# Kernel tuning notes

Measured on AMD Instinct MI355X. Metric: run time of the kernel, lower is better.

## Reference

```python
import jax, jax.numpy as jnp
import numpy as np

B = 128          # batch of codewords
M_CHK = 288      # n_check_nodes
N_VAR = 576      # n_variable_nodes
K_INFO = 288     # n_information_bits
N_ITER = 5
EDGE_P = 0.02    # ~11-12 edges per check row, LDPC-like sparsity


def setup_inputs() -> dict:
    key = jax.random.key(0)
    k1, k2, k3, k4 = jax.random.split(key, 4)
    inputs = jax.random.normal(k1, (B, N_VAR), dtype=jnp.float32)
    # sparse binary parity-check matrix, batched (keras RNN constants carry batch dim)
    H = jax.random.bernoulli(k2, EDGE_P, (B, M_CHK, N_VAR)).astype(jnp.float32)
    sigma2 = 0.5 + 0.5 * jax.random.uniform(k3, (B, 1), dtype=jnp.float32)
    # learned parameters
    input_ponderation = jnp.ones((N_ITER, 1), dtype=jnp.float32)
    out_ponderation = jnp.ones((N_ITER, 1), dtype=jnp.float32)
    skip_ponderation = jnp.ones((1, 1), dtype=jnp.float32)
    # per-edge check-to-variable weights of the neural BP cell
    w_cv = 1.0 + 0.02 * jax.random.normal(k4, (M_CHK, N_VAR), dtype=jnp.float32)
    gate_logit = jnp.asarray(0.0, dtype=jnp.float32)
    return {"inputs": inputs, "H": H, "sigma2": sigma2,
            "input_ponderation": input_ponderation,
            "out_ponderation": out_ponderation,
            "skip_ponderation": skip_ponderation,
            "w_cv": w_cv, "gate_logit": gate_logit}


def _decode(inputs, H, sigma2, input_ponderation, out_ponderation,
            skip_ponderation, w_cv, gate_logit):
    llrs = -4.0 * inputs / sigma2                                    # [B, n]
    # trainable=True path: normalize by mean |llr|
    norm_llrs = llrs / jnp.mean(jnp.abs(llrs), axis=-1, keepdims=True)
    # tile over iterations and apply input ponderation -> [B, T, n]
    x = norm_llrs[:, None, :] * input_ponderation

    mask = H                                                         # [B, m, n]
    gate = jax.nn.sigmoid(gate_logit)

    def cell(Mstate, x_t):
        # variable-to-check extrinsic messages on edges
        S = jnp.sum(Mstate, axis=1, keepdims=True)                   # [B, 1, n]
        V = (x_t[:, None, :] + S - Mstate) * mask                    # [B, m, n]
        # tanh-product check-node update (product excluding self via divide)
        t = jnp.tanh(0.5 * jnp.clip(V, -15.0, 15.0))
        t_edge = jnp.where(mask > 0, t, 1.0)
        P = jnp.prod(t_edge, axis=-1, keepdims=True)                 # [B, m, 1]
        t_safe = jnp.where(jnp.abs(t_edge) < 1e-7,
                           jnp.where(t_edge >= 0, 1e-7, -1e-7), t_edge)
        r = jnp.clip(P / t_safe, -1.0 + 1e-6, 1.0 - 1e-6)
        M_new = 2.0 * jnp.arctanh(r) * w_cv * mask                   # weighted c2v
        # gated (damped) state update
        M_out = gate * M_new + (1.0 - gate) * Mstate
        posterior = x_t + jnp.sum(M_out, axis=1)                     # [B, n]
        return M_out, posterior

    M0 = jnp.zeros_like(H)
    xs = jnp.swapaxes(x, 0, 1)                                       # [T, B, n]
    _, posts = jax.lax.scan(cell, M0, xs)
    outputs = jnp.swapaxes(posts, 0, 1)                              # [B, T, n]

    # post-normalization per iteration, weighted pooling over iterations
    norm_out = outputs / jnp.mean(jnp.abs(outputs), axis=-1, keepdims=True)
    pooled = jnp.mean(out_ponderation * norm_out, axis=-2)           # [B, n]
    out = pooled + skip_ponderation * norm_llrs                      # [1,1] broadcast
    return jax.nn.sigmoid(-out[:, :K_INFO])


def reference(inputs, H, sigma2, input_ponderation, out_ponderation,
              skip_ponderation, w_cv, gate_logit):
    return _decode(inputs, H, sigma2, input_ponderation, out_ponderation,
                   skip_ponderation, w_cv, gate_logit)
```

## Files before the change

### kernel.cpp

```cpp
#include <hip/hip_runtime.h>
#include <hip/hip_bf16.h>

#define B_SZ 128
#define MCHK 288
#define NVAR 576
#define KINFO 288
#define NITER 5
#define CAP 40
#define LCAP 3712
#define TPB 1024

__global__ __launch_bounds__(256) void build_edges(const float* __restrict__ H,
                                                   int* __restrict__ cntG,
                                                   unsigned short* __restrict__ idxG) {
    int row  = blockIdx.x * 4 + (threadIdx.x >> 6);
    int lane = threadIdx.x & 63;
    const float* hrow = H + (size_t)row * NVAR;
    const float4* h4  = (const float4*)hrow;
    float4 a = h4[lane];
    float4 bq = h4[64 + lane];
    float  c = hrow[512 + lane];
    int cnt = (a.x!=0.f)+(a.y!=0.f)+(a.z!=0.f)+(a.w!=0.f)
            + (bq.x!=0.f)+(bq.y!=0.f)+(bq.z!=0.f)+(bq.w!=0.f) + (c!=0.f);
    int pre = cnt;
    #pragma unroll
    for (int o = 1; o < 64; o <<= 1) {
        int n = __shfl_up(pre, o, 64);
        if (lane >= o) pre += n;
    }
    int p = pre - cnt;
    unsigned short* dst = idxG + (size_t)row * CAP;
    int base = lane * 4;
    if (a.x!=0.f)  { if (p<CAP) dst[p] = (unsigned short)(base    ); p++; }
    if (a.y!=0.f)  { if (p<CAP) dst[p] = (unsigned short)(base + 1); p++; }
    if (a.z!=0.f)  { if (p<CAP) dst[p] = (unsigned short)(base + 2); p++; }
    if (a.w!=0.f)  { if (p<CAP) dst[p] = (unsigned short)(base + 3); p++; }
    if (bq.x!=0.f) { if (p<CAP) dst[p] = (unsigned short)(256 + base    ); p++; }
    if (bq.y!=0.f) { if (p<CAP) dst[p] = (unsigned short)(256 + base + 1); p++; }
    if (bq.z!=0.f) { if (p<CAP) dst[p] = (unsigned short)(256 + base + 2); p++; }
    if (bq.w!=0.f) { if (p<CAP) dst[p] = (unsigned short)(256 + base + 3); p++; }
    if (c!=0.f)    { if (p<CAP) dst[p] = (unsigned short)(512 + lane);     p++; }
    if (lane == 63) cntG[row] = (pre > CAP) ? CAP : pre;
}

__global__ __launch_bounds__(TPB) void decode(
    const float* __restrict__ inp,   const float* __restrict__ sigma2,
    const float* __restrict__ ipond, const float* __restrict__ opond,
    const float* __restrict__ skipp, const float* __restrict__ wcv,
    const float* __restrict__ gatel, const int* __restrict__ cntG,
    const unsigned short* __restrict__ idxG, float* __restrict__ out) {

    __shared__ float xln[NVAR];
    __shared__ float S[NVAR];
    __shared__ float pooled[NVAR];
    __shared__ float Prow[MCHK];
    __shared__ float Mld[LCAP];
    __shared__ float tld[LCAP];
    __shared__ unsigned int ev[LCAP];
    __shared__ int   rcnt[MCHK];
    __shared__ int   roff[MCHK];
    __shared__ float red[16];
    __shared__ float scal;
    __shared__ int   EtotS;

    const int b    = blockIdx.x;
    const int tid  = threadIdx.x;
    const int wid  = tid >> 6;
    const int lane = tid & 63;

    const float sig  = sigma2[b];
    const float gate = 1.0f / (1.0f + __expf(-gatel[0]));
    const float gbar = 1.0f - gate;
    const float skip = skipp[0];

    float l = 0.0f, al = 0.0f;
    if (tid < NVAR) { l = -4.0f * inp[(size_t)b * NVAR + tid] / sig; al = fabsf(l); }
    #pragma unroll
    for (int o = 32; o; o >>= 1) al += __shfl_down(al, o, 64);
    if (lane == 0) red[wid] = al;

    int* sc = (int*)tld;
    if (tid < 512) {
        int cc = 0;
        if (tid < MCHK) { cc = cntG[b * MCHK + tid]; rcnt[tid] = cc; }
        sc[tid] = cc;
    }
    __syncthreads();
    if (tid == 0) {
        float s = 0.0f;
        #pragma unroll
        for (int i = 0; i < 16; ++i) s += red[i];
        scal = (float)NVAR / s;
    }
    __syncthreads();
    if (tid < NVAR) {
        xln[tid]    = l * scal;
        pooled[tid] = 0.0f;
        S[tid]      = 0.0f;
    }
    for (int d = 1; d < 512; d <<= 1) {
        int v = 0;
        if (tid < 512) v = sc[tid] + ((tid >= d) ? sc[tid - d] : 0);
        __syncthreads();
        if (tid < 512) sc[tid] = v;
        __syncthreads();
    }
    if (tid < MCHK) {
        int c = rcnt[tid];
        int o = sc[tid] - c;
        if (o >= LCAP)            { o = 0; c = 0; }
        else if (o + c > LCAP)    { c = LCAP - o; }
        roff[tid] = o; rcnt[tid] = c;
        const unsigned short* ig = idxG + ((size_t)b * MCHK + tid) * CAP;
        for (int j = 0; j < c; ++j) {
            int v = ig[j];
            ev[o + j]  = ((unsigned)tid << 16) | (unsigned)v;
            Mld[o + j] = 0.0f;
        }
    }
    if (tid == 0) EtotS = (sc[MCHK - 1] > LCAP) ? LCAP : sc[MCHK - 1];
    __syncthreads();
    const int E = EtotS;

    float ipl[NITER], opl[NITER];
    #pragma unroll
    for (int t = 0; t < NITER; ++t) { ipl[t] = ipond[t]; opl[t] = opond[t]; }

    for (int t = 0; t < NITER; ++t) {
        const float pt = ipl[t], ot = opl[t];

        for (int e = tid; e < E; e += TPB) {
            int v   = (int)(ev[e] & 0xFFFFu);
            float V = fmaf(pt, xln[v], S[v]) - Mld[e];
            V = fminf(15.0f, fmaxf(-15.0f, V));
            float ex = __expf(V);
            float te = (ex - 1.0f) * __builtin_amdgcn_rcpf(ex + 1.0f);
            float x  = 0.5f * V, x2 = x * x;
            float tp = x * fmaf(x2, fmaf(x2, fmaf(x2, -0.05396825f, 0.13333333f),
                                         -0.33333333f), 1.0f);
            tld[e] = (fabsf(V) < 0.5f) ? tp : te;
        }
        __syncthreads();

        if (tid < MCHK) {
            int c = rcnt[tid], o = roff[tid];
            float P = 1.0f;
            for (int j = 0; j < c; ++j) P *= tld[o + j];
            Prow[tid] = P;
        }
        if (tid < NVAR) S[tid] = 0.0f;
        __syncthreads();

        for (int e = tid; e < E; e += TPB) {
            unsigned pk = ev[e];
            int v = (int)(pk & 0xFFFFu);
            int m = (int)(pk >> 16);
            float tj = tld[e];
            float ts = (fabsf(tj) < 1e-7f) ? ((tj >= 0.0f) ? 1e-7f : -1e-7f) : tj;
            float r  = Prow[m] * __builtin_amdgcn_rcpf(ts);
            r = fminf(1.0f - 1e-6f, fmaxf(-1.0f + 1e-6f, r));
            float w  = wcv[m * NVAR + v];
            float Mn = __logf((1.0f + r) * __builtin_amdgcn_rcpf(1.0f - r)) * w;
            float Mo = fmaf(gate, Mn, gbar * Mld[e]);
            Mld[e] = Mo;
            atomicAdd(&S[v], Mo);
        }
        __syncthreads();

        float post = 0.0f, ap = 0.0f;
        if (tid < NVAR) { post = fmaf(pt, xln[tid], S[tid]); ap = fabsf(post); }
        #pragma unroll
        for (int o = 32; o; o >>= 1) ap += __shfl_down(ap, o, 64);
        if (lane == 0) red[wid] = ap;
        __syncthreads();
        if (tid == 0) {
            float s2 = 0.0f;
            #pragma unroll
            for (int i = 0; i < 16; ++i) s2 += red[i];
            scal = (float)NVAR / s2;
        }
        __syncthreads();
        if (tid < NVAR) pooled[tid] += ot * post * scal;
    }

    if (tid < KINFO) {
        float o = pooled[tid] * (1.0f / NITER) + skip * xln[tid];
        out[(size_t)b * KINFO + tid] = 1.0f / (1.0f + __expf(o));
    }
}

extern "C" void kernel_launch(void* const* d_in, const int* in_sizes, int n_in,
                              void* d_out, int out_size, void* d_ws, size_t ws_size,
                              hipStream_t stream) {
    const float* inp    = (const float*)d_in[0];
    const float* H      = (const float*)d_in[1];
    const float* sigma2 = (const float*)d_in[2];
    const float* ipond  = (const float*)d_in[3];
    const float* opond  = (const float*)d_in[4];
    const float* skipp  = (const float*)d_in[5];
    const float* wcv    = (const float*)d_in[6];
    const float* gatel  = (const float*)d_in[7];
    float* out = (float*)d_out;

    int* cntG = (int*)d_ws;
    unsigned short* idxG =
        (unsigned short*)((char*)d_ws + (size_t)B_SZ * MCHK * sizeof(int));

    build_edges<<<(B_SZ * MCHK) / 4, 256, 0, stream>>>(H, cntG, idxG);
    decode<<<B_SZ, TPB, 0, stream>>>(inp, sigma2, ipond, opond, skipp,
                                     wcv, gatel, cntG, idxG, out);
}
```

Before: 172.2 us.

## Split each codeword across two blocks with grid barrier and fused edge extraction

Removes the separate edge-building kernel and extracts edges from H inside the decode kernel using wave ballots, caching per-edge w_cv weights in shared memory. Each codeword's check rows are split across two blocks (256 blocks total), which exchange partial variable sums through global memory each iteration via a two-level grid-wide atomic barrier. This aims to double parallelism and cut launch and global gather costs. It relies on all 256 blocks being co-resident to avoid deadlock and adds barrier latency every iteration.

Result: slower. 254.8 us (+47.9%).

```diff
diff --git a/kernel.cpp b/kernel.cpp
--- a/kernel.cpp
+++ b/kernel.cpp
@@ -1,137 +1,126 @@
 #include <hip/hip_runtime.h>
-#include <hip/hip_bf16.h>
-
-#define B_SZ 128
-#define MCHK 288
-#define NVAR 576
+
+#define B_SZ  128
+#define MCHK  288
+#define NVAR  576
 #define KINFO 288
 #define NITER 5
-#define CAP 40
-#define LCAP 3712
-#define TPB 1024
-
-__global__ __launch_bounds__(256) void build_edges(const float* __restrict__ H,
-                                                   int* __restrict__ cntG,
-                                                   unsigned short* __restrict__ idxG) {
-    int row  = blockIdx.x * 4 + (threadIdx.x >> 6);
-    int lane = threadIdx.x & 63;
-    const float* hrow = H + (size_t)row * NVAR;
-    const float4* h4  = (const float4*)hrow;
-    float4 a = h4[lane];
-    float4 bq = h4[64 + lane];
-    float  c = hrow[512 + lane];
-    int cnt = (a.x!=0.f)+(a.y!=0.f)+(a.z!=0.f)+(a.w!=0.f)
-            + (bq.x!=0.f)+(bq.y!=0.f)+(bq.z!=0.f)+(bq.w!=0.f) + (c!=0.f);
-    int pre = cnt;
-    #pragma unroll
-    for (int o = 1; o < 64; o <<= 1) {
-        int n = __shfl_up(pre, o, 64);
-        if (lane >= o) pre += n;
-    }
-    int p = pre - cnt;
-    unsigned short* dst = idxG + (size_t)row * CAP;
-    int base = lane * 4;
-    if (a.x!=0.f)  { if (p<CAP) dst[p] = (unsigned short)(base    ); p++; }
-    if (a.y!=0.f)  { if (p<CAP) dst[p] = (unsigned short)(base + 1); p++; }
-    if (a.z!=0.f)  { if (p<CAP) dst[p] = (unsigned short)(base + 2); p++; }
-    if (a.w!=0.f)  { if (p<CAP) dst[p] = (unsigned short)(base + 3); p++; }
-    if (bq.x!=0.f) { if (p<CAP) dst[p] = (unsigned short)(256 + base    ); p++; }
-    if (bq.y!=0.f) { if (p<CAP) dst[p] = (unsigned short)(256 + base + 1); p++; }
-    if (bq.z!=0.f) { if (p<CAP) dst[p] = (unsigned short)(256 + base + 2); p++; }
-    if (bq.w!=0.f) { if (p<CAP) dst[p] = (unsigned short)(256 + base + 3); p++; }
-    if (c!=0.f)    { if (p<CAP) dst[p] = (unsigned short)(512 + lane);     p++; }
-    if (lane == 63) cntG[row] = (pre > CAP) ? CAP : pre;
-}
+#define MH    144
+#define ECAP  2048
+#define TPB   1024
 
 __global__ __launch_bounds__(TPB) void decode(
-    const float* __restrict__ inp,   const float* __restrict__ sigma2,
-    const float* __restrict__ ipond, const float* __restrict__ opond,
-    const float* __restrict__ skipp, const float* __restrict__ wcv,
-    const float* __restrict__ gatel, const int* __restrict__ cntG,
-    const unsigned short* __restrict__ idxG, float* __restrict__ out) {
-
+    const float* __restrict__ inp,   const float* __restrict__ H,
+    const float* __restrict__ sigma2,const float* __restrict__ ipond,
+    const float* __restrict__ opond, const float* __restrict__ skipp,
+    const float* __restrict__ wcv,   const float* __restrict__ gatel,
+    float* __restrict__ Sg, int* __restrict__ bar, float* __restrict__ out)
+{
+    __shared__ float Mld[ECAP];
+    __shared__ float tld[ECAP];
+    __shared__ float wld[ECAP];
+    __shared__ unsigned int ev[ECAP];
     __shared__ float xln[NVAR];
-    __shared__ float S[NVAR];
-    __shared__ float pooled[NVAR];
-    __shared__ float Prow[MCHK];
-    __shared__ float Mld[LCAP];
-    __shared__ float tld[LCAP];
-    __shared__ unsigned int ev[LCAP];
-    __shared__ int   rcnt[MCHK];
-    __shared__ int   roff[MCHK];
+    __shared__ float xs[NVAR];
+    __shared__ float Spart[NVAR];
+    __shared__ float pooled[KINFO];
+    __shared__ float Prow[MH];
+    __shared__ int   rcnt[MH], roff[MH];
     __shared__ float red[16];
-    __shared__ float scal;
-    __shared__ int   EtotS;
-
-    const int b    = blockIdx.x;
+    __shared__ float scalS;
+    __shared__ int   Ecnt;
+
+    const int bid  = blockIdx.x;
+    const int b    = bid >> 1;
+    const int grp  = bid & 1;
     const int tid  = threadIdx.x;
     const int wid  = tid >> 6;
     const int lane = tid & 63;
+    const int rlo  = grp * MH;
 
     const float sig  = sigma2[b];
     const float gate = 1.0f / (1.0f + __expf(-gatel[0]));
     const float gbar = 1.0f - gate;
-    const float skip = skipp[0];
+
+    float ipl[NITER], opl[NITER];
+    #pragma unroll
+    for (int t = 0; t < NITER; ++t) { ipl[t] = ipond[t]; opl[t] = opond[t]; }
 
     float l = 0.0f, al = 0.0f;
     if (tid < NVAR) { l = -4.0f * inp[(size_t)b * NVAR + tid] / sig; al = fabsf(l); }
     #pragma unroll
     for (int o = 32; o; o >>= 1) al += __shfl_down(al, o, 64);
     if (lane == 0) red[wid] = al;
-
-    int* sc = (int*)tld;
-    if (tid < 512) {
-        int cc = 0;
-        if (tid < MCHK) { cc = cntG[b * MCHK + tid]; rcnt[tid] = cc; }
-        sc[tid] = cc;
-    }
+    if (tid == 0) Ecnt = 0;
     __syncthreads();
     if (tid == 0) {
         float s = 0.0f;
         #pragma unroll
         for (int i = 0; i < 16; ++i) s += red[i];
-        scal = (float)NVAR / s;
+        scalS = (float)NVAR / s;
     }
     __syncthreads();
     if (tid < NVAR) {
-        xln[tid]    = l * scal;
-        pooled[tid] = 0.0f;
-        S[tid]      = 0.0f;
-    }
-    for (int d = 1; d < 512; d <<= 1) {
-        int v = 0;
-        if (tid < 512) v = sc[tid] + ((tid >= d) ? sc[tid - d] : 0);
-        __syncthreads();
-        if (tid < 512) sc[tid] = v;
-        __syncthreads();
-    }
-    if (tid < MCHK) {
-        int c = rcnt[tid];
-        int o = sc[tid] - c;
-        if (o >= LCAP)            { o = 0; c = 0; }
-        else if (o + c > LCAP)    { c = LCAP - o; }
-        roff[tid] = o; rcnt[tid] = c;
-        const unsigned short* ig = idxG + ((size_t)b * MCHK + tid) * CAP;
-        for (int j = 0; j < c; ++j) {
-            int v = ig[j];
-            ev[o + j]  = ((unsigned)tid << 16) | (unsigned)v;
-            Mld[o + j] = 0.0f;
-        }
-    }
-    if (tid == 0) EtotS = (sc[MCHK - 1] > LCAP) ? LCAP : sc[MCHK - 1];
+        float xv = l * scalS;
+        xln[tid] = xv;
+        xs[tid]  = ipl[0] * xv;
+    }
+    if (tid < KINFO) pooled[tid] = 0.0f;
+
+    {
+        const float* Hb = H + ((size_t)b * MCHK + rlo) * NVAR;
+        const unsigned long long lt = (1ull << lane) - 1ull;
+        for (int i = 0; i < MH / 16; ++i) {
+            int lr = wid + 16 * i;
+            const float* hr = Hb + (size_t)lr * NVAR;
+            const float4* h4 = (const float4*)hr;
+            float4 a  = h4[lane];
+            float4 b4 = h4[64 + lane];
+            float  c  = hr[512 + lane];
+            unsigned long long mk[9];
+            mk[0]=__ballot(a.x!=0.f);  mk[1]=__ballot(a.y!=0.f);
+            mk[2]=__ballot(a.z!=0.f);  mk[3]=__ballot(a.w!=0.f);
+            mk[4]=__ballot(b4.x!=0.f); mk[5]=__ballot(b4.y!=0.f);
+            mk[6]=__ballot(b4.z!=0.f); mk[7]=__ballot(b4.w!=0.f);
+            mk[8]=__ballot(c!=0.f);
+            int tot = 0;
+            #pragma unroll
+            for (int k = 0; k < 9; ++k) tot += __popcll(mk[k]);
+            int o0 = 0;
+            if (lane == 0) o0 = atomicAdd(&Ecnt, tot);
+            o0 = __shfl(o0, 0, 64);
+            int cc = (o0 >= ECAP) ? 0 : ((o0 + tot > ECAP) ? (ECAP - o0) : tot);
+            if (lane == 0) { roff[lr] = o0; rcnt[lr] = cc; }
+            const float* wrow = wcv + (size_t)(rlo + lr) * NVAR;
+            int base = 0;
+            #pragma unroll
+            for (int k = 0; k < 9; ++k) {
+                bool nz = (mk[k] >> lane) & 1ull;
+                int col = (k < 4) ? (4 * lane + k)
+                        : (k < 8) ? (256 + 4 * lane + (k - 4))
+                                  : (512 + lane);
+                if (nz) {
+                    int p = base + __popcll(mk[k] & lt);
+                    if (p < cc) {
+                        int e = o0 + p;
+                        ev[e]  = ((unsigned)lr << 16) | (unsigned)col;
+                        wld[e] = wrow[col];
+                        Mld[e] = 0.0f;
+                    }
+                }
+                base += __popcll(mk[k]);
+            }
+        }
+    }
     __syncthreads();
-    const int E = EtotS;
-
-    float ipl[NITER], opl[NITER];
-    #pragma unroll
-    for (int t = 0; t < NITER; ++t) { ipl[t] = ipond[t]; opl[t] = opond[t]; }
+    const int E1 = (Ecnt > ECAP) ? ECAP : Ecnt;
 
     for (int t = 0; t < NITER; ++t) {
         const float pt = ipl[t], ot = opl[t];
 
-        for (int e = tid; e < E; e += TPB) {
+        for (int e = tid; e < E1; e += TPB) {
             int v   = (int)(ev[e] & 0xFFFFu);
-            float V = fmaf(pt, xln[v], S[v]) - Mld[e];
+            float V = xs[v] - Mld[e];
             V = fminf(15.0f, fmaxf(-15.0f, V));
             float ex = __expf(V);
             float te = (ex - 1.0f) * __builtin_amdgcn_rcpf(ex + 1.0f);
@@ -142,49 +131,86 @@
         }
         __syncthreads();
 
-        if (tid < MCHK) {
+        if (tid < MH) {
             int c = rcnt[tid], o = roff[tid];
             float P = 1.0f;
             for (int j = 0; j < c; ++j) P *= tld[o + j];
             Prow[tid] = P;
         }
-        if (tid < NVAR) S[tid] = 0.0f;
-        __syncthreads();
-
-        for (int e = tid; e < E; e += TPB) {
+        if (tid < NVAR) Spart[tid] = 0.0f;
+        __syncthreads();
+
+        for (int e = tid; e < E1; e += TPB) {
             unsigned pk = ev[e];
-            int v = (int)(pk & 0xFFFFu);
-            int m = (int)(pk >> 16);
+            int v  = (int)(pk & 0xFFFFu);
+            int lr = (int)(pk >> 16);
             float tj = tld[e];
             float ts = (fabsf(tj) < 1e-7f) ? ((tj >= 0.0f) ? 1e-7f : -1e-7f) : tj;
-            float r  = Prow[m] * __builtin_amdgcn_rcpf(ts);
+            float r  = Prow[lr] * __builtin_amdgcn_rcpf(ts);
             r = fminf(1.0f - 1e-6f, fmaxf(-1.0f + 1e-6f, r));
-            float w  = wcv[m * NVAR + v];
-            float Mn = __logf((1.0f + r) * __builtin_amdgcn_rcpf(1.0f - r)) * w;
+            float Mn = __logf((1.0f + r) * __builtin_amdgcn_rcpf(1.0f - r)) * wld[e];
             float Mo = fmaf(gate, Mn, gbar * Mld[e]);
             Mld[e] = Mo;
-            atomicAdd(&S[v], Mo);
-        }
+            atomicAdd(&Spart[v], Mo);
+        }
+        __syncthreads();
+
+        const int par = t & 1;
+        float*       myS = Sg + (((size_t)par * B_SZ + b) * 2 + grp) * NVAR;
+        const float* otS = Sg + (((size_t)par * B_SZ + b) * 2 + (grp ^ 1)) * NVAR;
+        if (tid < NVAR)
+            __hip_atomic_store(&myS[tid], Spart[tid],
+                               __ATOMIC_RELAXED, __HIP_MEMORY_SCOPE_AGENT);
+        const bool wait = !(grp == 1 && t == NITER - 1);
+        __syncthreads();
+
+        int* leafp = bar + (t * 9 + (bid >> 5)) * 16;
+        int* rootp = bar + (t * 9 + 8) * 16;
+        if (tid == 0) {
+            __hip_atomic_fetch_add(leafp, 1, __ATOMIC_RELEASE, __HIP_MEMORY_SCOPE_AGENT);
+            if ((bid & 31) == 0) {
+                while (__hip_atomic_load(leafp, __ATOMIC_ACQUIRE,
+                                         __HIP_MEMORY_SCOPE_AGENT) < 32)
+                    __builtin_amdgcn_s_sleep(1);
+                __hip_atomic_fetch_add(rootp, 1, __ATOMIC_RELEASE, __HIP_MEMORY_SCOPE_AGENT);
+            }
+            if (wait)
+                while (__hip_atomic_load(rootp, __ATOMIC_ACQUIRE,
+                                         __HIP_MEMORY_SCOPE_AGENT) < 8)
+                    __builtin_amdgcn_s_sleep(1);
+        }
+        if (!wait) return;
         __syncthreads();
 
         float post = 0.0f, ap = 0.0f;
-        if (tid < NVAR) { post = fmaf(pt, xln[tid], S[tid]); ap = fabsf(post); }
-        #pragma unroll
-        for (int o = 32; o; o >>= 1) ap += __shfl_down(ap, o, 64);
-        if (lane == 0) red[wid] = ap;
-        __syncthreads();
-        if (tid == 0) {
-            float s2 = 0.0f;
+        const float ptn = (t < NITER - 1) ? ipl[t + 1] : 0.0f;
+        if (tid < NVAR) {
+            float rs = __hip_atomic_load(&otS[tid], __ATOMIC_RELAXED,
+                                         __HIP_MEMORY_SCOPE_AGENT);
+            float s2 = Spart[tid] + rs;
+            xs[tid]  = fmaf(ptn, xln[tid], s2);
+            post = fmaf(pt, xln[tid], s2);
+            ap   = fabsf(post);
+        }
+        if (grp == 0) {
             #pragma unroll
-            for (int i = 0; i < 16; ++i) s2 += red[i];
-            scal = (float)NVAR / s2;
-        }
-        __syncthreads();
-        if (tid < NVAR) pooled[tid] += ot * post * scal;
+            for (int o = 32; o; o >>= 1) ap += __shfl_down(ap, o, 64);
+            if (lane == 0) red[wid] = ap;
+            __syncthreads();
+            if (tid == 0) {
+                float s = 0.0f;
+                #pragma unroll
+                for (int i = 0; i < 16; ++i) s += red[i];
+                scalS = (float)NVAR / s;
+            }
+            __syncthreads();
+            if (tid < KINFO) pooled[tid] += ot * post * scalS;
+        }
+        __syncthreads();
     }
 
     if (tid < KINFO) {
-        float o = pooled[tid] * (1.0f / NITER) + skip * xln[tid];
+        float o = pooled[tid] * (1.0f / NITER) + skipp[0] * xln[tid];
         out[(size_t)b * KINFO + tid] = 1.0f / (1.0f + __expf(o));
     }
 }
@@ -202,11 +228,10 @@
     const float* gatel  = (const float*)d_in[7];
     float* out = (float*)d_out;
 
-    int* cntG = (int*)d_ws;
-    unsigned short* idxG =
-        (unsigned short*)((char*)d_ws + (size_t)B_SZ * MCHK * sizeof(int));
-
-    build_edges<<<(B_SZ * MCHK) / 4, 256, 0, stream>>>(H, cntG, idxG);
-    decode<<<B_SZ, TPB, 0, stream>>>(inp, sigma2, ipond, opond, skipp,
-                                     wcv, gatel, cntG, idxG, out);
+    float* Sg = (float*)d_ws;
+    int*   bar = (int*)((char*)d_ws + (size_t)2 * B_SZ * 2 * NVAR * sizeof(float));
+
+    hipMemsetAsync(bar, 0, NITER * 9 * 16 * sizeof(int), stream);
+    decode<<<2 * B_SZ, TPB, 0, stream>>>(inp, H, sigma2, ipond, opond, skipp,
+                                         wcv, gatel, Sg, bar, out);
 }
```
